# Performance work log

Measured on AMD Instinct MI355X. Metric: run time of the kernel, lower is better.

## Reference

```python
import jax, jax.numpy as jnp
import numpy as np

N, E, B = 16384, 65536, 32
D_IN, ED, H, L = 4, 5, 64, 3  # node feat, edge feat, hidden=output, num layers
NEG_SLOPE = 0.1
EPS = 1e-5


def _leaky(v):
    return jnp.where(v > 0, v, NEG_SLOPE * v)


def setup_inputs() -> dict:
    key = jax.random.key(0)
    ks = jax.random.split(key, 32)
    s = 0.05
    inp = {
        'x': jax.random.normal(ks[0], (N, D_IN), jnp.float32),
        'edge_index': jax.random.randint(ks[1], (2, E), 0, N),
        'edge_attr': jax.random.normal(ks[2], (E, ED), jnp.float32),
        'batch': jnp.sort(jax.random.randint(ks[3], (N,), 0, B)),
        # input projection Linear(4 -> H)
        'W_in': s * jax.random.normal(ks[4], (H, D_IN), jnp.float32),
        'b_in': jnp.zeros((H,), jnp.float32),
        # per-layer edge MLP: Linear(ED->H), Linear(H->H), Linear(H->H*H); stacked over L
        'ew1': s * jax.random.normal(ks[5], (L, H, ED), jnp.float32),
        'eb1': jnp.zeros((L, H), jnp.float32),
        'ew2': s * jax.random.normal(ks[6], (L, H, H), jnp.float32),
        'eb2': jnp.zeros((L, H), jnp.float32),
        'ew3': s * jax.random.normal(ks[7], (L, H * H, H), jnp.float32),
        'eb3': jnp.zeros((L, H * H), jnp.float32),
        # NNConv root weight + bias per layer
        'root_w': s * jax.random.normal(ks[8], (L, H, H), jnp.float32),
        'root_b': jnp.zeros((L, H), jnp.float32),
        # LayerNorm per layer
        'ln_g': jnp.ones((L, H), jnp.float32),
        'ln_b': jnp.zeros((L, H), jnp.float32),
        # prediction head: Linear(H->H), Linear(H->H//2), Linear(H//2->1)
        'pw1': s * jax.random.normal(ks[9], (H, H), jnp.float32),
        'pb1': jnp.zeros((H,), jnp.float32),
        'pw2': s * jax.random.normal(ks[10], (H // 2, H), jnp.float32),
        'pb2': jnp.zeros((H // 2,), jnp.float32),
        'pw3': s * jax.random.normal(ks[11], (1, H // 2), jnp.float32),
        'pb3': jnp.zeros((1,), jnp.float32),
    }
    return inp


def reference(x, edge_index, edge_attr, batch, W_in, b_in, ew1, eb1, ew2, eb2,
              ew3, eb3, root_w, root_b, ln_g, ln_b, pw1, pb1, pw2, pb2, pw3, pb3):
    src, dst = edge_index[0], edge_index[1]
    n_nodes = x.shape[0]
    n_edges = edge_attr.shape[0]
    # in-degree for scatter-mean (PyG yields 0 for isolated nodes)
    deg = jax.ops.segment_sum(jnp.ones((n_edges,), x.dtype), dst, num_segments=n_nodes)
    deg = jnp.maximum(deg, 1.0)[:, None]

    # input projection (dropout = identity in eval)
    h = _leaky(x @ W_in.T + b_in)

    for l in range(L):
        # edge MLP -> per-edge weight matrix [E, H, H]
        e = _leaky(edge_attr @ ew1[l].T + eb1[l])
        e = _leaky(e @ ew2[l].T + eb2[l])
        Wf = (e @ ew3[l].T + eb3[l]).reshape(n_edges, H, H)
        # message = x_src @ W_edge, scatter-mean to dst
        msg = jnp.einsum('ei,eio->eo', h[src], Wf)
        agg = jax.ops.segment_sum(msg, dst, num_segments=n_nodes) / deg
        out = agg + h @ root_w[l].T + root_b[l]
        # LayerNorm (post-norm)
        mu = out.mean(-1, keepdims=True)
        var = ((out - mu) ** 2).mean(-1, keepdims=True)
        out = (out - mu) * jax.lax.rsqrt(var + EPS) * ln_g[l] + ln_b[l]
        # activation + (identity) dropout + residual (in==out for all layers)
        h = _leaky(out) + h

    # global mean pool over graphs
    pooled = jax.ops.segment_sum(h, batch, num_segments=B)
    cnt = jax.ops.segment_sum(jnp.ones((n_nodes,), h.dtype), batch, num_segments=B)
    pooled = pooled / jnp.maximum(cnt, 1.0)[:, None]

    # prediction head
    p = _leaky(pooled @ pw1.T + pb1)
    p = _leaky(p @ pw2.T + pb2)
    pred = (p @ pw3.T + pb3).squeeze(-1)  # [B]
    return pred
```

## Files before the change

kernel.cpp:

```cpp
#include <hip/hip_runtime.h>
#include <hip/hip_bf16.h>

#define N_NODES 16384
#define N_EDGES 65536
#define NB      32
#define H       64
#define NLAYERS 3
#define NEG     0.1f
#define LN_EPS  1e-5f

typedef _Float16 f16;
typedef _Float16 f16x2 __attribute__((ext_vector_type(2)));
typedef _Float16 f16x8 __attribute__((ext_vector_type(8)));
typedef __fp16   hf16x2 __attribute__((ext_vector_type(2)));
typedef float    f32x16 __attribute__((ext_vector_type(16)));

union F16x8 { f16x8 v; f16x2 p[4]; int4 i4; int2 i2[2]; };
union F16x2U { f16x2 h2; hf16x2 raw; unsigned int u; };
union F16U   { f16 h; unsigned short u; };

__device__ __forceinline__ f16x2 pkrtz(float a, float b) {
    F16x2U t; t.raw = __builtin_amdgcn_cvt_pkrtz(a, b); return t.h2;
}
__device__ __forceinline__ float leaky(float v) { return v > 0.f ? v : NEG * v; }

__global__ __launch_bounds__(256) void k_init(const float* __restrict__ x,
                                              const float* __restrict__ Win,
                                              const float* __restrict__ bin,
                                              const int* __restrict__ dst,
                                              float* __restrict__ h,
                                              float* __restrict__ deg) {
    int bid = blockIdx.x;
    if (bid < 4096) {
        int t = bid * 256 + threadIdx.x;
        int n = t >> 6, j = t & 63;
        const float* xr = x + n * 4;
        const float* wr = Win + j * 4;
        float v = bin[j] + xr[0] * wr[0] + xr[1] * wr[1] + xr[2] * wr[2] + xr[3] * wr[3];
        h[t] = leaky(v);
    } else {
        int e = (bid - 4096) * 256 + threadIdx.x;
        atomicAdd(&deg[dst[e]], 1.0f);
    }
}

__global__ __launch_bounds__(256) void k_prep_bp(const float* __restrict__ ew3,
                                                 const float* __restrict__ eb3,
                                                 f16* __restrict__ Bp) {
    int tg    = blockIdx.x * 256 + threadIdx.x;
    int lane  = tg & 63;
    int gslot = tg >> 6;
    int l     = gslot / 520;
    int slot  = gslot - l * 520;
    const float* ew3l = ew3 + (size_t)l * 262144;
    const float* eb3l = eb3 + (size_t)l * 4096;
    int i   = slot >> 3;
    int rem = slot & 7;
    int ks  = rem >> 1;
    int oq  = rem & 1;
    int o   = oq * 32 + (lane & 31);
    int k0  = ks * 16 + (lane >> 5) * 8;
    float v[8];
    if (i < 64) {
        const float* s = ew3l + ((size_t)(i * 64 + o)) * 64 + k0;
        float4 a = ((const float4*)s)[0];
        float4 b = ((const float4*)s)[1];
        v[0] = a.x; v[1] = a.y; v[2] = a.z; v[3] = a.w;
        v[4] = b.x; v[5] = b.y; v[6] = b.z; v[7] = b.w;
    } else {
#pragma unroll
        for (int j = 0; j < 8; j++) v[j] = eb3l[(k0 + j) * 64 + o];
    }
    union { int4 i4; f16 a[8]; } out;
#pragma unroll
    for (int j = 0; j < 8; j++) out.a[j] = (f16)v[j];
    *(int4*)(Bp + (size_t)l * 266240 + (size_t)slot * 512 + lane * 8) = out.i4;
}

__global__ __launch_bounds__(256) void k_edge_mlp(const float* __restrict__ ea,
                                                  const float* __restrict__ w1,
                                                  const float* __restrict__ b1,
                                                  const float* __restrict__ w2,
                                                  const float* __restrict__ b2,
                                                  unsigned short* __restrict__ e2h) {
    __shared__ float eas[128 * 8];
    __shared__ __align__(16) unsigned short e1L[128 * 72];
    int t = threadIdx.x;
    int eb = blockIdx.x * 128;

    for (int idx = t; idx < 640; idx += 256) {
        int r = idx / 5, d = idx - r * 5;
        eas[r * 8 + d] = ea[(size_t)eb * 5 + idx];
    }
    __syncthreads();

    {
        int kk = t & 63;
        int eg = t >> 6;
        float w1r[5];
#pragma unroll
        for (int d = 0; d < 5; d++) w1r[d] = w1[kk * 5 + d];
        float b1r = b1[kk];
        for (int g = 0; g < 32; g++) {
            int row = g * 4 + eg;
            float4 a4 = *(const float4*)(eas + row * 8);
            float a5 = eas[row * 8 + 4];
            float v = b1r + a4.x * w1r[0] + a4.y * w1r[1] + a4.z * w1r[2] + a4.w * w1r[3] + a5 * w1r[4];
            F16U z; z.h = (f16)leaky(v);
            e1L[row * 72 + kk] = z.u;
        }
    }
    __syncthreads();

    int lane = t & 63;
    int w    = t >> 6;
    int eq2  = w >> 1, oq = w & 1;
    int m    = lane & 31;
    int kp   = lane >> 5;

    F16x8 Bf[4];
#pragma unroll
    for (int ks = 0; ks < 4; ks++) {
        const float* s = w2 + (size_t)(oq * 32 + m) * 64 + ks * 16 + kp * 8;
        float4 a = ((const float4*)s)[0];
        float4 b = ((const float4*)s)[1];
        Bf[ks].p[0] = pkrtz(a.x, a.y);
        Bf[ks].p[1] = pkrtz(a.z, a.w);
        Bf[ks].p[2] = pkrtz(b.x, b.y);
        Bf[ks].p[3] = pkrtz(b.z, b.w);
    }
    float b2r = b2[oq * 32 + m];

    f32x16 C0 = {0,0,0,0,0,0,0,0,0,0,0,0,0,0,0,0};
    f32x16 C1 = {0,0,0,0,0,0,0,0,0,0,0,0,0,0,0,0};
#pragma unroll
    for (int ks = 0; ks < 4; ks++) {
        int koff = (ks * 16 + kp * 8);
        F16x8 A0, A1;
        A0.i4 = *(const int4*)(e1L + (size_t)(eq2 * 64 + m) * 72 + koff);
        A1.i4 = *(const int4*)(e1L + (size_t)(eq2 * 64 + 32 + m) * 72 + koff);
        C0 = __builtin_amdgcn_mfma_f32_32x32x16_f16(A0.v, Bf[ks].v, C0, 0, 0, 0);
        C1 = __builtin_amdgcn_mfma_f32_32x32x16_f16(A1.v, Bf[ks].v, C1, 0, 0, 0);
    }

    int o = oq * 32 + m;
#pragma unroll
    for (int reg = 0; reg < 16; reg++) {
        int r = (reg & 3) + 8 * (reg >> 2) + 4 * kp;
        F16U z; z.h = (f16)leaky(C0[reg] + b2r);
        e2h[(size_t)(eb + eq2 * 64 + r) * 64 + o] = z.u;
    }
#pragma unroll
    for (int reg = 0; reg < 16; reg++) {
        int r = (reg & 3) + 8 * (reg >> 2) + 4 * kp;
        F16U z; z.h = (f16)leaky(C1[reg] + b2r);
        e2h[(size_t)(eb + eq2 * 64 + 32 + r) * 64 + o] = z.u;
    }
}

#define HS_STRIDE 76

__device__ __forceinline__ void loadB8(const f16* __restrict__ Bp, int c, int oq, int lane, F16x8* dstB) {
    const f16* base = Bp + (((size_t)(c * 16 + oq)) << 9) + lane * 8;
#pragma unroll
    for (int di = 0; di < 2; di++)
#pragma unroll
        for (int ks = 0; ks < 4; ks++)
            dstB[di * 4 + ks].i4 = *(const int4*)(base + ((di * 8 + ks * 2) << 9));
}
__device__ __forceinline__ void loadB4(const f16* __restrict__ Bp, int oq, int lane, F16x8* dstB) {
    const f16* base = Bp + (((size_t)(512 + oq)) << 9) + lane * 8;
#pragma unroll
    for (int ks = 0; ks < 4; ks++)
        dstB[ks].i4 = *(const int4*)(base + ((ks * 2) << 9));
}

__device__ __forceinline__ void msg_chunk(int c, const F16x8* Bc,
                                          const unsigned short* hp0, const unsigned short* hp1,
                                          const f16x2 (*e2p)[4][4], f32x16& C0, f32x16& C1) {
    unsigned int rr0 = *(const unsigned int*)(hp0 + 2 * c);
    unsigned int rr1 = *(const unsigned int*)(hp1 + 2 * c);
#pragma unroll
    for (int di = 0; di < 2; di++) {
        F16x2U hh0, hh1;
        unsigned int sel = di ? 0x03020302u : 0x01000100u;
        hh0.u = __builtin_amdgcn_perm(rr0, rr0, sel);
        hh1.u = __builtin_amdgcn_perm(rr1, rr1, sel);
#pragma unroll
        for (int ks = 0; ks < 4; ks++) {
            F16x8 A0, A1;
#pragma unroll
            for (int r = 0; r < 4; r++) {
                A0.p[r] = hh0.h2 * e2p[0][ks][r];
                A1.p[r] = hh1.h2 * e2p[1][ks][r];
            }
            C0 = __builtin_amdgcn_mfma_f32_32x32x16_f16(A0.v, Bc[di * 4 + ks].v, C0, 0, 0, 0);
            C1 = __builtin_amdgcn_mfma_f32_32x32x16_f16(A1.v, Bc[di * 4 + ks].v, C1, 0, 0, 0);
        }
    }
}

__global__ __launch_bounds__(256, 2) void k_msg(const float* __restrict__ h,
                                                const unsigned int* __restrict__ e2h,
                                                const f16* __restrict__ Bp,
                                                const int* __restrict__ src,
                                                const int* __restrict__ dst,
                                                float* __restrict__ agg) {
    __shared__ __align__(16) unsigned short hsL[128 * HS_STRIDE];
    __shared__ int dstL[128];

    const int t    = threadIdx.x;
    const int lane = t & 63;
    const int w    = t >> 6;
    const int eq2  = w >> 1, oq = w & 1;
    const int m    = lane & 31;
    const int kp   = lane >> 5;
    const int eb   = blockIdx.x * 128;

    {
        int e    = t >> 1;
        int half = t & 1;
        int nsrc = src[eb + e];
        const float4* hr = (const float4*)(h + (size_t)nsrc * 64 + half * 32);
        unsigned int* hrow = (unsigned int*)hsL + e * (HS_STRIDE / 2) + half * 16;
#pragma unroll
        for (int q = 0; q < 8; q++) {
            float4 v = hr[q];
            F16x2U p0, p1;
            p0.raw = __builtin_amdgcn_cvt_pkrtz(v.x, v.y);
            p1.raw = __builtin_amdgcn_cvt_pkrtz(v.z, v.w);
            hrow[q * 2 + 0] = p0.u;
            hrow[q * 2 + 1] = p1.u;
        }
        if (t < 128) dstL[t] = dst[eb + t];
    }

    f16x2 e2p[2][4][4];
#pragma unroll
    for (int et = 0; et < 2; et++) {
        const unsigned int* row = e2h + (size_t)(eb + eq2 * 64 + et * 32 + m) * 32;
#pragma unroll
        for (int ks = 0; ks < 4; ks++) {
            int4 q = *(const int4*)(row + ks * 8 + kp * 4);
            F16x2U u0, u1, u2, u3;
            u0.u = q.x; u1.u = q.y; u2.u = q.z; u3.u = q.w;
            e2p[et][ks][0] = u0.h2; e2p[et][ks][1] = u1.h2;
            e2p[et][ks][2] = u2.h2; e2p[et][ks][3] = u3.h2;
        }
    }
    __syncthreads();

    f32x16 C0 = {0,0,0,0,0,0,0,0,0,0,0,0,0,0,0,0};
    f32x16 C1 = {0,0,0,0,0,0,0,0,0,0,0,0,0,0,0,0};

    const unsigned short* hp0 = hsL + (eq2 * 64 + m) * HS_STRIDE;
    const unsigned short* hp1 = hp0 + 32 * HS_STRIDE;

    F16x8 B0[8], B1[8], B2[8];
    loadB8(Bp, 0, oq, lane, B0);
    loadB8(Bp, 1, oq, lane, B1);
    int c = 0;
    for (int it = 0; it < 10; it++) {
        loadB8(Bp, c + 2, oq, lane, B2); msg_chunk(c, B0, hp0, hp1, e2p, C0, C1); c++;
        loadB8(Bp, c + 2, oq, lane, B0); msg_chunk(c, B1, hp0, hp1, e2p, C0, C1); c++;
        loadB8(Bp, c + 2, oq, lane, B1); msg_chunk(c, B2, hp0, hp1, e2p, C0, C1); c++;
    }
    loadB4(Bp, oq, lane, B2);
    msg_chunk(30, B0, hp0, hp1, e2p, C0, C1);
    msg_chunk(31, B1, hp0, hp1, e2p, C0, C1);
#pragma unroll
    for (int ks = 0; ks < 4; ks++) {
        int koff = (ks * 16 + kp * 8) * 2;
        const char* r0p = (const char*)hsL + (size_t)(eq2 * 64 + m) * (HS_STRIDE * 2) + koff;
        const char* r1p = r0p + 32 * (HS_STRIDE * 2);
        F16x8 A0, A1;
        A0.i2[0] = *(const int2*)(r0p); A0.i2[1] = *(const int2*)(r0p + 8);
        A1.i2[0] = *(const int2*)(r1p); A1.i2[1] = *(const int2*)(r1p + 8);
        C0 = __builtin_amdgcn_mfma_f32_32x32x16_f16(A0.v, B2[ks].v, C0, 0, 0, 0);
        C1 = __builtin_amdgcn_mfma_f32_32x32x16_f16(A1.v, B2[ks].v, C1, 0, 0, 0);
    }

    int o = oq * 32 + m;
#pragma unroll
    for (int reg = 0; reg < 16; reg++) {
        int r = (reg & 3) + 8 * (reg >> 2) + 4 * kp;
        atomicAdd(&agg[(size_t)dstL[eq2 * 64 + r] * 64 + o], C0[reg]);
    }
#pragma unroll
    for (int reg = 0; reg < 16; reg++) {
        int r = (reg & 3) + 8 * (reg >> 2) + 4 * kp;
        atomicAdd(&agg[(size_t)dstL[eq2 * 64 + 32 + r] * 64 + o], C1[reg]);
    }
}

__global__ __launch_bounds__(256) void k_node(const float* __restrict__ agg,
                                              const float* __restrict__ deg,
                                              const float* __restrict__ rw,
                                              const float* __restrict__ rb,
                                              const float* __restrict__ lg,
                                              const float* __restrict__ lb,
                                              float* __restrict__ h) {
    __shared__ float rws[64][65];
    __shared__ float hrow[4][64];
    int t = threadIdx.x;
    for (int idx = t; idx < 4096; idx += 256) rws[idx >> 6][idx & 63] = rw[idx];
    int g = t >> 6, j = t & 63;
    int n = blockIdx.x * 4 + g;
    float hv = h[(size_t)n * 64 + j];
    hrow[g][j] = hv;
    __syncthreads();
    float v = rb[j] + agg[(size_t)n * 64 + j] / fmaxf(deg[n], 1.0f);
#pragma unroll 8
    for (int i = 0; i < 64; i++) v += hrow[g][i] * rws[j][i];
    float mu = v;
#pragma unroll
    for (int msk = 32; msk > 0; msk >>= 1) mu += __shfl_xor(mu, msk);
    mu *= (1.f / 64.f);
    float d = v - mu;
    float var = d * d;
#pragma unroll
    for (int msk = 32; msk > 0; msk >>= 1) var += __shfl_xor(var, msk);
    var *= (1.f / 64.f);
    float ov = d * rsqrtf(var + LN_EPS) * lg[j] + lb[j];
    h[(size_t)n * 64 + j] = leaky(ov) + hv;
}

__global__ __launch_bounds__(256) void k_pool(const float* __restrict__ h,
                                              const int* __restrict__ batch,
                                              float* __restrict__ pooled,
                                              float* __restrict__ cnt) {
    int t = threadIdx.x;
    int g = t >> 6, j = t & 63;
    int n0 = blockIdx.x * 32 + g * 8;
    int cur = batch[n0];
    float acc = 0.f, cacc = 0.f;
    for (int q = 0; q < 8; q++) {
        int n = n0 + q;
        int b = batch[n];
        float v = h[(size_t)n * 64 + j];
        if (b != cur) {
            atomicAdd(&pooled[cur * 64 + j], acc);
            if (j == 0) atomicAdd(&cnt[cur], cacc);
            acc = 0.f; cacc = 0.f; cur = b;
        }
        acc += v; cacc += 1.f;
    }
    atomicAdd(&pooled[cur * 64 + j], acc);
    if (j == 0) atomicAdd(&cnt[cur], cacc);
}

__global__ __launch_bounds__(256) void k_head(const float* __restrict__ pooled,
                                              const float* __restrict__ cnt,
                                              const float* __restrict__ pw1, const float* __restrict__ pb1,
                                              const float* __restrict__ pw2, const float* __restrict__ pb2,
                                              const float* __restrict__ pw3, const float* __restrict__ pb3,
                                              float* __restrict__ out) {
    __shared__ float ps[32][64];
    __shared__ float p1[32][64];
    __shared__ float p2[32][32];
    int t = threadIdx.x;
    for (int idx = t; idx < 2048; idx += 256) {
        int b = idx >> 6, j = idx & 63;
        ps[b][j] = pooled[idx] / fmaxf(cnt[b], 1.0f);
    }
    __syncthreads();
    for (int idx = t; idx < 2048; idx += 256) {
        int b = idx >> 6, j = idx & 63;
        float v = pb1[j];
#pragma unroll 8
        for (int i = 0; i < 64; i++) v += ps[b][i] * pw1[j * 64 + i];
        p1[b][j] = leaky(v);
    }
    __syncthreads();
    for (int idx = t; idx < 1024; idx += 256) {
        int b = idx >> 5, j = idx & 31;
        float v = pb2[j];
#pragma unroll 8
        for (int i = 0; i < 64; i++) v += p1[b][i] * pw2[j * 64 + i];
        p2[b][j] = leaky(v);
    }
    __syncthreads();
    if (t < 32) {
        float v = pb3[0];
#pragma unroll 8
        for (int i = 0; i < 32; i++) v += p2[t][i] * pw3[i];
        out[t] = v;
    }
}

extern "C" void kernel_launch(void* const* d_in, const int* in_sizes, int n_in,
                              void* d_out, int out_size, void* d_ws, size_t ws_size,
                              hipStream_t stream) {
    const float* x    = (const float*)d_in[0];
    const int*   eidx = (const int*)  d_in[1];
    const float* ea   = (const float*)d_in[2];
    const int*   bat  = (const int*)  d_in[3];
    const float* Win  = (const float*)d_in[4];
    const float* bin  = (const float*)d_in[5];
    const float* ew1  = (const float*)d_in[6];
    const float* eb1  = (const float*)d_in[7];
    const float* ew2  = (const float*)d_in[8];
    const float* eb2  = (const float*)d_in[9];
    const float* ew3  = (const float*)d_in[10];
    const float* eb3  = (const float*)d_in[11];
    const float* rw   = (const float*)d_in[12];
    const float* rb   = (const float*)d_in[13];
    const float* lg   = (const float*)d_in[14];
    const float* lb   = (const float*)d_in[15];
    const float* pw1  = (const float*)d_in[16];
    const float* pb1  = (const float*)d_in[17];
    const float* pw2  = (const float*)d_in[18];
    const float* pb2  = (const float*)d_in[19];
    const float* pw3  = (const float*)d_in[20];
    const float* pb3  = (const float*)d_in[21];
    float* out = (float*)d_out;

    float* ws     = (float*)d_ws;
    float* h      = ws;
    float* agg    = ws + 1048576;
    float* deg    = ws + 4194304;
    float* pooled = ws + 4210688;
    float* cnt    = ws + 4212736;
    unsigned int* e2h = (unsigned int*)(ws + 4212800);
    f16* Bp       = (f16*)(ws + 4212800 + 2097152);

    const int* srcp = eidx;
    const int* dstp = eidx + N_EDGES;

    (void)hipMemsetAsync(agg, 0, (size_t)(3164224) * sizeof(float), stream);

    k_init   <<<4352, 256, 0, stream>>>(x, Win, bin, dstp, h, deg);
    k_prep_bp<<<390, 256, 0, stream>>>(ew3, eb3, Bp);

    for (int l = 0; l < NLAYERS; l++) {
        float* agg_l = agg + (size_t)l * N_NODES * H;
        k_edge_mlp<<<N_EDGES / 128, 256, 0, stream>>>(ea, ew1 + l * 320, eb1 + l * 64,
                                                      ew2 + l * 4096, eb2 + l * 64,
                                                      (unsigned short*)e2h);
        k_msg     <<<N_EDGES / 128, 256, 0, stream>>>(h, e2h, Bp + (size_t)l * 266240,
                                                      srcp, dstp, agg_l);
        k_node    <<<N_NODES / 4, 256, 0, stream>>>(agg_l, deg, rw + l * 4096, rb + l * 64,
                                                    lg + l * 64, lb + l * 64, h);
    }

    k_pool<<<N_NODES / 32, 256, 0, stream>>>(h, bat, pooled, cnt);
    k_head<<<1, 256, 0, stream>>>(pooled, cnt, pw1, pb1, pw2, pb2, pw3, pb3, out);
}
```

Before: 369.6 us.

## Split message K-range across two blocks, MFMA node update with fused pooling

After: 409.3 us. 1.11x slower.

```diff
diff --git a/kernel.cpp b/kernel.cpp
--- a/kernel.cpp
+++ b/kernel.cpp
@@ -200,7 +200,7 @@
     }
 }
 
-__global__ __launch_bounds__(256, 2) void k_msg(const float* __restrict__ h,
+__global__ __launch_bounds__(256, 4) void k_msg(const float* __restrict__ h,
                                                 const unsigned int* __restrict__ e2h,
                                                 const f16* __restrict__ Bp,
                                                 const int* __restrict__ src,
@@ -215,7 +215,9 @@
     const int eq2  = w >> 1, oq = w & 1;
     const int m    = lane & 31;
     const int kp   = lane >> 5;
-    const int eb   = blockIdx.x * 128;
+    const int by   = blockIdx.x & 1;
+    const int eb   = (blockIdx.x >> 1) * 128;
+    const int cb   = by * 16;
 
     {
         int e    = t >> 1;
@@ -257,27 +259,33 @@
     const unsigned short* hp1 = hp0 + 32 * HS_STRIDE;
 
     F16x8 B0[8], B1[8], B2[8];
-    loadB8(Bp, 0, oq, lane, B0);
-    loadB8(Bp, 1, oq, lane, B1);
-    int c = 0;
-    for (int it = 0; it < 10; it++) {
+    loadB8(Bp, cb + 0, oq, lane, B0);
+    loadB8(Bp, cb + 1, oq, lane, B1);
+    int c = cb;
+    for (int it = 0; it < 4; it++) {
         loadB8(Bp, c + 2, oq, lane, B2); msg_chunk(c, B0, hp0, hp1, e2p, C0, C1); c++;
         loadB8(Bp, c + 2, oq, lane, B0); msg_chunk(c, B1, hp0, hp1, e2p, C0, C1); c++;
         loadB8(Bp, c + 2, oq, lane, B1); msg_chunk(c, B2, hp0, hp1, e2p, C0, C1); c++;
     }
-    loadB4(Bp, oq, lane, B2);
-    msg_chunk(30, B0, hp0, hp1, e2p, C0, C1);
-    msg_chunk(31, B1, hp0, hp1, e2p, C0, C1);
-#pragma unroll
-    for (int ks = 0; ks < 4; ks++) {
-        int koff = (ks * 16 + kp * 8) * 2;
-        const char* r0p = (const char*)hsL + (size_t)(eq2 * 64 + m) * (HS_STRIDE * 2) + koff;
-        const char* r1p = r0p + 32 * (HS_STRIDE * 2);
-        F16x8 A0, A1;
-        A0.i2[0] = *(const int2*)(r0p); A0.i2[1] = *(const int2*)(r0p + 8);
-        A1.i2[0] = *(const int2*)(r1p); A1.i2[1] = *(const int2*)(r1p + 8);
-        C0 = __builtin_amdgcn_mfma_f32_32x32x16_f16(A0.v, B2[ks].v, C0, 0, 0, 0);
-        C1 = __builtin_amdgcn_mfma_f32_32x32x16_f16(A1.v, B2[ks].v, C1, 0, 0, 0);
+    loadB8(Bp, cb + 14, oq, lane, B2);
+    msg_chunk(cb + 12, B0, hp0, hp1, e2p, C0, C1);
+    loadB8(Bp, cb + 15, oq, lane, B0);
+    msg_chunk(cb + 13, B1, hp0, hp1, e2p, C0, C1);
+    if (by) loadB4(Bp, oq, lane, B1);
+    msg_chunk(cb + 14, B2, hp0, hp1, e2p, C0, C1);
+    msg_chunk(cb + 15, B0, hp0, hp1, e2p, C0, C1);
+    if (by) {
+#pragma unroll
+        for (int ks = 0; ks < 4; ks++) {
+            int koff = (ks * 16 + kp * 8) * 2;
+            const char* r0p = (const char*)hsL + (size_t)(eq2 * 64 + m) * (HS_STRIDE * 2) + koff;
+            const char* r1p = r0p + 32 * (HS_STRIDE * 2);
+            F16x8 A0, A1;
+            A0.i2[0] = *(const int2*)(r0p); A0.i2[1] = *(const int2*)(r0p + 8);
+            A1.i2[0] = *(const int2*)(r1p); A1.i2[1] = *(const int2*)(r1p + 8);
+            C0 = __builtin_amdgcn_mfma_f32_32x32x16_f16(A0.v, B1[ks].v, C0, 0, 0, 0);
+            C1 = __builtin_amdgcn_mfma_f32_32x32x16_f16(A1.v, B1[ks].v, C1, 0, 0, 0);
+        }
     }
 
     int o = oq * 32 + m;
@@ -299,69 +307,120 @@
                                               const float* __restrict__ rb,
                                               const float* __restrict__ lg,
                                               const float* __restrict__ lb,
-                                              float* __restrict__ h) {
-    __shared__ float rws[64][65];
-    __shared__ float hrow[4][64];
-    int t = threadIdx.x;
-    for (int idx = t; idx < 4096; idx += 256) rws[idx >> 6][idx & 63] = rw[idx];
-    int g = t >> 6, j = t & 63;
-    int n = blockIdx.x * 4 + g;
-    float hv = h[(size_t)n * 64 + j];
-    hrow[g][j] = hv;
-    __syncthreads();
-    float v = rb[j] + agg[(size_t)n * 64 + j] / fmaxf(deg[n], 1.0f);
-#pragma unroll 8
-    for (int i = 0; i < 64; i++) v += hrow[g][i] * rws[j][i];
-    float mu = v;
-#pragma unroll
-    for (int msk = 32; msk > 0; msk >>= 1) mu += __shfl_xor(mu, msk);
-    mu *= (1.f / 64.f);
-    float d = v - mu;
-    float var = d * d;
-#pragma unroll
-    for (int msk = 32; msk > 0; msk >>= 1) var += __shfl_xor(var, msk);
-    var *= (1.f / 64.f);
-    float ov = d * rsqrtf(var + LN_EPS) * lg[j] + lb[j];
-    h[(size_t)n * 64 + j] = leaky(ov) + hv;
-}
-
-__global__ __launch_bounds__(256) void k_pool(const float* __restrict__ h,
+                                              float* __restrict__ h,
                                               const int* __restrict__ batch,
                                               float* __restrict__ pooled,
-                                              float* __restrict__ cnt) {
+                                              int last) {
+    __shared__ __align__(16) unsigned short hA[64 * 72];
+    __shared__ float outL[64][68];
     int t = threadIdx.x;
-    int g = t >> 6, j = t & 63;
-    int n0 = blockIdx.x * 32 + g * 8;
-    int cur = batch[n0];
-    float acc = 0.f, cacc = 0.f;
-    for (int q = 0; q < 8; q++) {
-        int n = n0 + q;
-        int b = batch[n];
-        float v = h[(size_t)n * 64 + j];
-        if (b != cur) {
-            atomicAdd(&pooled[cur * 64 + j], acc);
-            if (j == 0) atomicAdd(&cnt[cur], cacc);
-            acc = 0.f; cacc = 0.f; cur = b;
-        }
-        acc += v; cacc += 1.f;
-    }
-    atomicAdd(&pooled[cur * 64 + j], acc);
-    if (j == 0) atomicAdd(&cnt[cur], cacc);
+    int nb = blockIdx.x * 64;
+    int lane = t & 63, w = t >> 6;
+    int nq = w >> 1, oq = w & 1;
+    int m = lane & 31, kp = lane >> 5;
+
+    {
+        int r = t >> 2, c0 = (t & 3) * 16;
+        const float4* hr = (const float4*)(h + (size_t)(nb + r) * 64 + c0);
+        unsigned int* drow = (unsigned int*)hA + r * 36 + c0 / 2;
+#pragma unroll
+        for (int q = 0; q < 4; q++) {
+            float4 v = hr[q];
+            F16x2U p0, p1;
+            p0.raw = __builtin_amdgcn_cvt_pkrtz(v.x, v.y);
+            p1.raw = __builtin_amdgcn_cvt_pkrtz(v.z, v.w);
+            drow[q * 2] = p0.u; drow[q * 2 + 1] = p1.u;
+        }
+    }
+    F16x8 Bf[4];
+#pragma unroll
+    for (int ks = 0; ks < 4; ks++) {
+        const float* s = rw + (size_t)(oq * 32 + m) * 64 + ks * 16 + kp * 8;
+        float4 a = ((const float4*)s)[0];
+        float4 b = ((const float4*)s)[1];
+        Bf[ks].p[0] = pkrtz(a.x, a.y);
+        Bf[ks].p[1] = pkrtz(a.z, a.w);
+        Bf[ks].p[2] = pkrtz(b.x, b.y);
+        Bf[ks].p[3] = pkrtz(b.z, b.w);
+    }
+    __syncthreads();
+
+    f32x16 C = {0,0,0,0,0,0,0,0,0,0,0,0,0,0,0,0};
+#pragma unroll
+    for (int ks = 0; ks < 4; ks++) {
+        F16x8 A;
+        A.i4 = *(const int4*)(hA + (size_t)(nq * 32 + m) * 72 + ks * 16 + kp * 8);
+        C = __builtin_amdgcn_mfma_f32_32x32x16_f16(A.v, Bf[ks].v, C, 0, 0, 0);
+    }
+
+    int o = oq * 32 + m;
+#pragma unroll
+    for (int reg = 0; reg < 16; reg++) {
+        int r = (reg & 3) + 8 * (reg >> 2) + 4 * kp;
+        int n = nq * 32 + r;
+        outL[n][o] = C[reg] + rb[o] + agg[(size_t)(nb + n) * 64 + o] / fmaxf(deg[nb + n], 1.0f);
+    }
+    __syncthreads();
+
+    float gj = lg[lane], bj = lb[lane];
+    float accp = 0.f;
+    int cur = batch[nb + w * 16];
+    for (int q = 0; q < 16; q++) {
+        int n = w * 16 + q;
+        float v = outL[n][lane];
+        float mu = v;
+#pragma unroll
+        for (int msk = 32; msk > 0; msk >>= 1) mu += __shfl_xor(mu, msk);
+        mu *= (1.f / 64.f);
+        float d = v - mu;
+        float var = d * d;
+#pragma unroll
+        for (int msk = 32; msk > 0; msk >>= 1) var += __shfl_xor(var, msk);
+        var *= (1.f / 64.f);
+        float ov = d * rsqrtf(var + LN_EPS) * gj + bj;
+        float hn = leaky(ov) + h[(size_t)(nb + n) * 64 + lane];
+        h[(size_t)(nb + n) * 64 + lane] = hn;
+        if (last) {
+            int b = batch[nb + n];
+            if (b != cur) { atomicAdd(&pooled[cur * 64 + lane], accp); accp = 0.f; cur = b; }
+            accp += hn;
+        }
+    }
+    if (last) atomicAdd(&pooled[cur * 64 + lane], accp);
 }
 
 __global__ __launch_bounds__(256) void k_head(const float* __restrict__ pooled,
-                                              const float* __restrict__ cnt,
+                                              const int* __restrict__ batch,
                                               const float* __restrict__ pw1, const float* __restrict__ pb1,
                                               const float* __restrict__ pw2, const float* __restrict__ pb2,
                                               const float* __restrict__ pw3, const float* __restrict__ pb3,
                                               float* __restrict__ out) {
+    __shared__ float cntL[32];
     __shared__ float ps[32][64];
     __shared__ float p1[32][64];
     __shared__ float p2[32][32];
     int t = threadIdx.x;
+    if (t < 32) cntL[t] = 0.f;
+    __syncthreads();
+    {
+        const int4* bp4 = (const int4*)(batch + t * 64);
+        int cur = batch[t * 64];
+        float c = 0.f;
+        for (int q = 0; q < 16; q++) {
+            int4 b4 = bp4[q];
+            int bs[4] = { b4.x, b4.y, b4.z, b4.w };
+#pragma unroll
+            for (int e = 0; e < 4; e++) {
+                if (bs[e] != cur) { atomicAdd(&cntL[cur], c); cur = bs[e]; c = 0.f; }
+                c += 1.f;
+            }
+        }
+        atomicAdd(&cntL[cur], c);
+    }
+    __syncthreads();
     for (int idx = t; idx < 2048; idx += 256) {
         int b = idx >> 6, j = idx & 63;
-        ps[b][j] = pooled[idx] / fmaxf(cnt[b], 1.0f);
+        ps[b][j] = pooled[idx] / fmaxf(cntL[b], 1.0f);
     }
     __syncthreads();
     for (int idx = t; idx < 2048; idx += 256) {
@@ -420,14 +479,13 @@
     float* agg    = ws + 1048576;
     float* deg    = ws + 4194304;
     float* pooled = ws + 4210688;
-    float* cnt    = ws + 4212736;
     unsigned int* e2h = (unsigned int*)(ws + 4212800);
     f16* Bp       = (f16*)(ws + 4212800 + 2097152);
 
     const int* srcp = eidx;
     const int* dstp = eidx + N_EDGES;
 
-    (void)hipMemsetAsync(agg, 0, (size_t)(3164224) * sizeof(float), stream);
+    (void)hipMemsetAsync(agg, 0, (size_t)3164224 * sizeof(float), stream);
 
     k_init   <<<4352, 256, 0, stream>>>(x, Win, bin, dstp, h, deg);
     k_prep_bp<<<390, 256, 0, stream>>>(ew3, eb3, Bp);
@@ -437,12 +495,12 @@
         k_edge_mlp<<<N_EDGES / 128, 256, 0, stream>>>(ea, ew1 + l * 320, eb1 + l * 64,
                                                       ew2 + l * 4096, eb2 + l * 64,
                                                       (unsigned short*)e2h);
-        k_msg     <<<N_EDGES / 128, 256, 0, stream>>>(h, e2h, Bp + (size_t)l * 266240,
-                                                      srcp, dstp, agg_l);
-        k_node    <<<N_NODES / 4, 256, 0, stream>>>(agg_l, deg, rw + l * 4096, rb + l * 64,
-                                                    lg + l * 64, lb + l * 64, h);
-    }
-
-    k_pool<<<N_NODES / 32, 256, 0, stream>>>(h, bat, pooled, cnt);
-    k_head<<<1, 256, 0, stream>>>(pooled, cnt, pw1, pb1, pw2, pb2, pw3, pb3, out);
-}
+        k_msg     <<<N_EDGES / 64, 256, 0, stream>>>(h, e2h, Bp + (size_t)l * 266240,
+                                                     srcp, dstp, agg_l);
+        k_node    <<<N_NODES / 64, 256, 0, stream>>>(agg_l, deg, rw + l * 4096, rb + l * 64,
+                                                     lg + l * 64, lb + l * 64, h,
+                                                     bat, pooled, l == NLAYERS - 1 ? 1 : 0);
+    }
+
+    k_head<<<1, 256, 0, stream>>>(pooled, bat, pw1, pb1, pw2, pb2, pw3, pb3, out);
+}
```
